# Optimization experiments

Hardware: AMD Instinct MI355X
Metric: run time of the kernel (lower is better)

## Reference

```python
import jax, jax.numpy as jnp
import numpy as np

D = 128            # shared state dim for path/link/queue (required equal by scatter_nd)
T = 8              # message-passing iterations
NUM_POLICIES = 3
MAX_NUM_QUEUES = 3
READOUT = 256


def gru(x, h, W, U, b):
    # Keras GRUCell, reset_after=True. W:[F,3D], U:[D,3D], b:[2,3D]
    gi = x @ W + b[0]
    gh = h @ U + b[1]
    iz, ir, ih = jnp.split(gi, 3, axis=-1)
    hz, hr, hh = jnp.split(gh, 3, axis=-1)
    z = jax.nn.sigmoid(iz + hz)
    r = jax.nn.sigmoid(ir + hr)
    cand = jnp.tanh(ih + r * hh)
    return z * h + (1.0 - z) * cand


def masked_gru_rnn(x_seq, h0, W, U, b):
    # x_seq: [N, Tm, F]; Masking layer: skip timesteps whose features are all zero
    def step(h, xt):
        mask = jnp.any(xt != 0, axis=-1, keepdims=True)
        hn = gru(xt, h, W, U, b)
        return jnp.where(mask, hn, h), None
    h, _ = jax.lax.scan(step, h0, jnp.swapaxes(x_seq, 0, 1))
    return h


def setup_inputs() -> dict:
    rng = np.random.default_rng(0)
    N_PATHS, N_LINKS, L, QL = 20000, 4000, 8, 3
    N_QUEUES = N_LINKS * QL
    E = N_PATHS * L
    f32 = np.float32
    traffic = rng.random(N_PATHS, dtype=f32)
    packets = rng.random(N_PATHS, dtype=f32)
    capacity = rng.random(N_LINKS, dtype=f32)
    weight = rng.random(N_QUEUES, dtype=f32)
    policy = rng.integers(0, NUM_POLICIES, N_LINKS).astype(np.int32)
    priority = rng.integers(0, MAX_NUM_QUEUES, N_QUEUES).astype(np.int32)
    # each path traverses L links; hop positions are unique per path (scatter_nd well-defined)
    path_ids = np.repeat(np.arange(N_PATHS, dtype=np.int32), L)
    l_q_p = np.tile(np.arange(L, dtype=np.int32), N_PATHS)
    l_p_s = l_q_p.copy()
    link_to_path = rng.integers(0, N_LINKS, E).astype(np.int32)
    queue_to_path = (link_to_path * QL + rng.integers(0, QL, E)).astype(np.int32)
    path_to_queue = path_ids.copy()
    sequence_queues = queue_to_path.copy()
    queue_to_link = np.arange(N_QUEUES, dtype=np.int32)  # queue i belongs to link i//QL
    sequence_links = np.repeat(np.arange(N_LINKS, dtype=np.int32), QL)
    l_q_l = np.tile(np.arange(QL, dtype=np.int32), N_LINKS)

    def p(k, *shape):
        kk = jax.random.fold_in(jax.random.key(0), k)
        return jax.random.normal(kk, shape, jnp.float32) / np.sqrt(f32(shape[0]))

    params = dict(
        Wp=p(1, 2 * D, 3 * D), Up=p(2, D, 3 * D), bp=0.01 * p(3, 2, 3 * D),
        Wl=p(4, D, 3 * D), Ul=p(5, D, 3 * D), bl=0.01 * p(6, 2, 3 * D),
        Wq=p(7, D, 3 * D), Uq=p(8, D, 3 * D), bq=0.01 * p(9, 2, 3 * D),
        Wr1=p(10, D, READOUT), br1=jnp.zeros((READOUT,), jnp.float32),
        Wr2=p(11, READOUT, READOUT), br2=jnp.zeros((READOUT,), jnp.float32),
        Wr3=p(12, READOUT, 1), br3=jnp.zeros((1,), jnp.float32),
    )
    inp = dict(
        traffic=jnp.asarray(traffic), packets=jnp.asarray(packets),
        capacity=jnp.asarray(capacity), weight=jnp.asarray(weight),
        policy=jnp.asarray(policy), priority=jnp.asarray(priority),
        path_ids=jnp.asarray(path_ids), l_q_p=jnp.asarray(l_q_p), l_p_s=jnp.asarray(l_p_s),
        link_to_path=jnp.asarray(link_to_path), queue_to_path=jnp.asarray(queue_to_path),
        path_to_queue=jnp.asarray(path_to_queue), sequence_queues=jnp.asarray(sequence_queues),
        queue_to_link=jnp.asarray(queue_to_link), sequence_links=jnp.asarray(sequence_links),
        l_q_l=jnp.asarray(l_q_l), n_paths=N_PATHS, n_links=N_LINKS, n_queues=N_QUEUES,
    )
    inp.update(params)
    return inp


def reference(traffic, packets, capacity, weight, policy, priority, path_ids, l_q_p, l_p_s,
              link_to_path, queue_to_path, path_to_queue, sequence_queues, queue_to_link,
              sequence_links, l_q_l, n_paths, n_links, n_queues,
              Wp, Up, bp, Wl, Ul, bl, Wq, Uq, bq, Wr1, br1, Wr2, br2, Wr3, br3):
    path_state = jnp.concatenate([traffic[:, None], packets[:, None],
                                  jnp.zeros((n_paths, D - 2), jnp.float32)], axis=1)
    link_state = jnp.concatenate([capacity[:, None],
                                  jax.nn.one_hot(policy, NUM_POLICIES, dtype=jnp.float32),
                                  jnp.zeros((n_links, D - NUM_POLICIES - 1), jnp.float32)], axis=1)
    queue_state = jnp.concatenate([jax.nn.one_hot(priority, MAX_NUM_QUEUES, dtype=jnp.float32),
                                   weight[:, None],
                                   jnp.zeros((n_queues, D - MAX_NUM_QUEUES - 1), jnp.float32)], axis=1)
    max_p = int(np.asarray(l_q_p).max()) + 1
    max_l = int(np.asarray(l_q_l).max()) + 1
    for _ in range(T):
        # paths: gather link+queue states, scatter into padded sequences, run masked GRU
        qg = queue_state[queue_to_path]                       # [E, D]
        lg = link_state[link_to_path]                         # [E, D]
        qi = jnp.zeros((n_paths, max_p, D), jnp.float32).at[path_ids, l_q_p].add(qg)
        li = jnp.zeros((n_paths, max_p, D), jnp.float32).at[path_ids, l_p_s].add(lg)
        path_state = masked_gru_rnn(jnp.concatenate([qi, li], axis=2), path_state, Wp, Up, bp)
        # queues: sum path states per queue, single GRU cell step
        path_sum = jax.ops.segment_sum(path_state[path_to_queue], sequence_queues,
                                       num_segments=n_queues)
        queue_state = gru(path_sum, queue_state, Wq, Uq, bq)
        # links: gather queue states into padded sequences, masked GRU
        qi2 = jnp.zeros((n_links, max_l, D), jnp.float32).at[sequence_links, l_q_l].add(
            queue_state[queue_to_link])
        link_state = masked_gru_rnn(qi2, link_state, Wl, Ul, bl)
    h = jax.nn.relu(path_state @ Wr1 + br1)
    h = jax.nn.relu(h @ Wr2 + br2)
    return h @ Wr3 + br3
```

## Files before the change

kernel.cpp:

```cpp
#include <hip/hip_runtime.h>
#include <hip/hip_bf16.h>
#include <hip/hip_fp16.h>
#include <math.h>

#define NP 20000
#define NL 4000
#define NQ 12000
#define NE 160000
#define DD 128
#define N3 384
#define TT 8
#define FR 512

typedef __attribute__((ext_vector_type(8))) short bf16x8;
typedef __attribute__((ext_vector_type(4))) float f32x4;

__device__ float g_path [NP * DD];
__device__ float g_link [NL * DD];
__device__ float g_queue[NQ * DD];
__device__ unsigned short g_qgi_h[NQ * N3];
__device__ unsigned short g_lgi_h[NL * N3];
__device__ float g_psum [NQ * DD];
__device__ int   g_peq  [NE];
__device__ int   g_pel  [NE];
__device__ int   g_qlmap[NQ];
__device__ int   g_counts[NQ];
__device__ int   g_off  [NQ + 1];
__device__ int   g_cur  [NQ];
__device__ int   g_col  [NE];
__device__ int   g_nzq  [NQ];
__device__ int   g_nzl  [NL];
__device__ unsigned short g_upb_hi[24*4*FR], g_upb_lo[24*4*FR];
__device__ unsigned short g_wpb_hi[2*24*4*FR], g_wpb_lo[2*24*4*FR];
__device__ unsigned short g_wlb_hi[24*4*FR], g_wlb_lo[24*4*FR];
__device__ unsigned short g_wuq_hi[24*8*FR], g_wuq_lo[24*8*FR];
__device__ unsigned short g_ulb_hi[24*4*FR], g_ulb_lo[24*4*FR];
__device__ unsigned short g_w1b_hi[16*4*FR], g_w1b_lo[16*4*FR];
__device__ unsigned short g_w2b_hi[16*8*FR], g_w2b_lo[16*8*FR];

__device__ __forceinline__ float fsig(float x)  { return 1.0f / (1.0f + __expf(-x)); }
__device__ __forceinline__ float ftanh(float x) { return 2.0f / (1.0f + __expf(-2.0f * x)) - 1.0f; }

__device__ __forceinline__ void split_bf(float v, unsigned short& hi, unsigned short& lo) {
    unsigned u = __float_as_uint(v);
    hi = (unsigned short)(u >> 16);
    float lof = v - __uint_as_float(u & 0xFFFF0000u);
    lo = (unsigned short)(__float_as_uint(lof) >> 16);
}
__device__ __forceinline__ unsigned short f2h(float v) {
    __half h = __float2half_rn(v);
    return *reinterpret_cast<unsigned short*>(&h);
}
__device__ __forceinline__ float h2f(unsigned short u) {
    __half h = *reinterpret_cast<__half*>(&u);
    return __half2float(h);
}

__global__ void k_init_maps() {
    int i = blockIdx.x * 256 + threadIdx.x;
    if (i < NE) { g_peq[i] = -1; g_pel[i] = -1; }
    if (i < NQ) { g_qlmap[i] = -1; g_counts[i] = 0; }
}

__global__ void k_fill_maps(const int* __restrict__ path_ids, const int* __restrict__ l_q_p,
                            const int* __restrict__ l_p_s, const int* __restrict__ queue_to_path,
                            const int* __restrict__ link_to_path, const int* __restrict__ sequence_queues,
                            const int* __restrict__ sequence_links, const int* __restrict__ l_q_l,
                            const int* __restrict__ queue_to_link) {
    int i = blockIdx.x * 256 + threadIdx.x;
    if (i < NE) {
        int p = path_ids[i];
        g_peq[p * 8 + l_q_p[i]] = queue_to_path[i];
        g_pel[p * 8 + l_p_s[i]] = link_to_path[i];
        atomicAdd(&g_counts[sequence_queues[i]], 1);
    }
    if (i < NQ) {
        g_qlmap[sequence_links[i] * 3 + l_q_l[i]] = queue_to_link[i];
    }
}

__global__ __launch_bounds__(1024) void k_scan() {
    __shared__ int part[1024];
    int tid = threadIdx.x;
    int base = tid * 12;
    int local[12];
    int s = 0;
#pragma unroll
    for (int j = 0; j < 12; j++) {
        int idx = base + j;
        int v = (idx < NQ) ? g_counts[idx] : 0;
        local[j] = s; s += v;
    }
    part[tid] = s;
    __syncthreads();
    for (int off = 1; off < 1024; off <<= 1) {
        int v = (tid >= off) ? part[tid - off] : 0;
        __syncthreads();
        part[tid] += v;
        __syncthreads();
    }
    int pre = (tid > 0) ? part[tid - 1] : 0;
#pragma unroll
    for (int j = 0; j < 12; j++) {
        int idx = base + j;
        if (idx < NQ) { g_off[idx] = pre + local[j]; g_cur[idx] = pre + local[j]; }
    }
    if (tid == 1023) g_off[NQ] = part[1023];
}

__global__ void k_fill_csr(const int* __restrict__ sequence_queues, const int* __restrict__ path_to_queue) {
    int i = blockIdx.x * 256 + threadIdx.x;
    if (i < NE) {
        int q = sequence_queues[i];
        int pos = atomicAdd(&g_cur[q], 1);
        g_col[pos] = path_to_queue[i];
    }
}

__global__ void k_init_states(const float* __restrict__ traffic, const float* __restrict__ packets,
                              const float* __restrict__ capacity, const int* __restrict__ policy,
                              const float* __restrict__ weight, const int* __restrict__ priority) {
    int idx = blockIdx.x * 256 + threadIdx.x;
    if (idx < NP * DD) {
        int p = idx >> 7, d = idx & 127;
        g_path[idx] = (d == 0) ? traffic[p] : (d == 1) ? packets[p] : 0.0f;
    }
    if (idx < NL * DD) {
        int l = idx >> 7, d = idx & 127;
        float v = 0.0f;
        if (d == 0) v = capacity[l];
        else if (d >= 1 && d <= 3) v = (policy[l] == d - 1) ? 1.0f : 0.0f;
        g_link[idx] = v;
    }
    if (idx < NQ * DD) {
        int q = idx >> 7, d = idx & 127;
        float v = 0.0f;
        if (d < 3) v = (priority[q] == d) ? 1.0f : 0.0f;
        else if (d == 3) v = weight[q];
        g_queue[idx] = v;
    }
}

__global__ void k_pack(int mode, const float* __restrict__ W, int ldn) {
    unsigned short *dhi, *dlo;
    int nt_cnt, kc_cnt, kc_total, kc_base;
    if (mode == 0)      { dhi=g_upb_hi; dlo=g_upb_lo; nt_cnt=24; kc_cnt=4; kc_total=4; kc_base=0; }
    else if (mode == 1) { dhi=g_wpb_hi; dlo=g_wpb_lo; nt_cnt=24; kc_cnt=4; kc_total=4; kc_base=0; }
    else if (mode == 2) { dhi=g_wpb_hi+24*4*FR; dlo=g_wpb_lo+24*4*FR; nt_cnt=24; kc_cnt=4; kc_total=4; kc_base=0; }
    else if (mode == 3) { dhi=g_wlb_hi; dlo=g_wlb_lo; nt_cnt=24; kc_cnt=4; kc_total=4; kc_base=0; }
    else if (mode == 4) { dhi=g_wuq_hi; dlo=g_wuq_lo; nt_cnt=24; kc_cnt=4; kc_total=8; kc_base=0; }
    else if (mode == 5) { dhi=g_wuq_hi; dlo=g_wuq_lo; nt_cnt=24; kc_cnt=4; kc_total=8; kc_base=4; }
    else if (mode == 6) { dhi=g_ulb_hi; dlo=g_ulb_lo; nt_cnt=24; kc_cnt=4; kc_total=4; kc_base=0; }
    else if (mode == 7) { dhi=g_w1b_hi; dlo=g_w1b_lo; nt_cnt=16; kc_cnt=4; kc_total=4; kc_base=0; }
    else                { dhi=g_w2b_hi; dlo=g_w2b_lo; nt_cnt=16; kc_cnt=8; kc_total=8; kc_base=0; }
    int tot = nt_cnt * kc_cnt * FR;
    int idx = blockIdx.x * 256 + threadIdx.x;
    if (idx >= tot) return;
    int j = idx & 7, lane = (idx >> 3) & 63;
    int kc = (idx >> 9) % kc_cnt, nt = idx / (kc_cnt * FR);
    int k = kc * 32 + (lane >> 4) * 8 + j;
    int col = nt * 16 + (lane & 15);
    float v = W[(size_t)k * ldn + col];
    unsigned short hi, lo;
    split_bf(v, hi, lo);
    size_t o = ((size_t)(nt * kc_total + kc_base + kc)) * FR + (size_t)lane * 8 + j;
    dhi[o] = hi; dlo[o] = lo;
}

__global__ void k_nz(int mode) {
    const float* st = mode ? g_link : g_queue;
    int n = mode ? NL : NQ;
    int* outf = mode ? g_nzl : g_nzq;
    int w = threadIdx.x >> 6, lane = threadIdx.x & 63;
    int row = blockIdx.x * 4 + w;
    if (row < n) {
        const float* r = st + (size_t)row * DD;
        bool nz = (r[lane] != 0.0f) || (r[lane + 64] != 0.0f);
        unsigned long long b = __ballot(nz);
        if (lane == 0) outf[row] = (b != 0ULL) ? 1 : 0;
    }
}

__global__ __launch_bounds__(256) void k_gemm_mfma(int mode, const float* __restrict__ bias) {
    const float* A; unsigned short* C; const unsigned short *Bh, *Bl;
    int r0; bool useB;
    if (mode == 2) {
        A = g_queue; C = g_qgi_h; Bh = g_wlb_hi; Bl = g_wlb_lo;
        r0 = blockIdx.x * 16; useB = true;
    } else {
        if (blockIdx.x < NQ / 16) {
            A = g_queue; C = g_qgi_h; Bh = g_wpb_hi; Bl = g_wpb_lo;
            r0 = blockIdx.x * 16; useB = true;
        } else {
            A = g_link; C = g_lgi_h; Bh = g_wpb_hi + 24*4*FR; Bl = g_wpb_lo + 24*4*FR;
            r0 = (blockIdx.x - NQ / 16) * 16; useB = false;
        }
    }
    __shared__ unsigned short as_hi[16][136], as_lo[16][136];
    const int tid = threadIdx.x, w = tid >> 6, l = tid & 63;
    for (int idx = tid; idx < 16 * DD; idx += 256) {
        unsigned short hi, lo;
        split_bf(A[(size_t)r0 * DD + idx], hi, lo);
        as_hi[idx >> 7][idx & 127] = hi; as_lo[idx >> 7][idx & 127] = lo;
    }
    __syncthreads();
    f32x4 acc[6];
#pragma unroll
    for (int n = 0; n < 6; n++) acc[n] = (f32x4){0.f, 0.f, 0.f, 0.f};
#pragma unroll
    for (int kc = 0; kc < 4; kc++) {
        int kk = kc * 32 + (l >> 4) * 8;
        bf16x8 ah = *reinterpret_cast<const bf16x8*>(&as_hi[l & 15][kk]);
        bf16x8 al = *reinterpret_cast<const bf16x8*>(&as_lo[l & 15][kk]);
#pragma unroll
        for (int n = 0; n < 6; n++) {
            int nt = 6 * w + n;
            size_t boff = ((size_t)(nt * 4 + kc)) * FR + (size_t)l * 8;
            bf16x8 bhv = *reinterpret_cast<const bf16x8*>(&Bh[boff]);
            bf16x8 blv = *reinterpret_cast<const bf16x8*>(&Bl[boff]);
            acc[n] = __builtin_amdgcn_mfma_f32_16x16x32_bf16(ah, bhv, acc[n], 0, 0, 0);
            acc[n] = __builtin_amdgcn_mfma_f32_16x16x32_bf16(al, bhv, acc[n], 0, 0, 0);
            acc[n] = __builtin_amdgcn_mfma_f32_16x16x32_bf16(ah, blv, acc[n], 0, 0, 0);
        }
    }
    const int rbase = (l >> 4) * 4;
#pragma unroll
    for (int n = 0; n < 6; n++) {
        int col = (6 * w + n) * 16 + (l & 15);
        float bv = useB ? bias[col] : 0.f;
#pragma unroll
        for (int i = 0; i < 4; i++)
            C[(size_t)(r0 + rbase + i) * N3 + col] = f2h(acc[n][i] + bv);
    }
}

__global__ __launch_bounds__(256) void k_path(const float* __restrict__ bp) {
    __shared__ unsigned short hs_hi[2][16][136];
    __shared__ unsigned short hs_lo[2][16][136];
    __shared__ int qqA[8][16], llA[8][16], mAsh[8][16];
    const int tid = threadIdx.x;
    const int w = tid >> 6, l = tid & 63;
    const int r0 = blockIdx.x * 16;
    if (tid < 128) {
        int r = tid >> 3, t = tid & 7;
        int e = (r0 + r) * 8 + t;
        int qq = g_peq[e], ll = g_pel[e];
        qqA[t][r] = qq; llA[t][r] = ll;
        mAsh[t][r] = (g_nzq[qq] | g_nzl[ll]);
    }
    const int c0 = 32 * w + (l & 15), c1 = c0 + 16;
    const int rbase = (l >> 4) * 4;
    float h0[4], h1[4];
#pragma unroll
    for (int i = 0; i < 4; i++) {
        h0[i] = g_path[(size_t)(r0 + rbase + i) * DD + c0];
        h1[i] = g_path[(size_t)(r0 + rbase + i) * DD + c1];
    }
#pragma unroll
    for (int i = 0; i < 4; i++) {
        unsigned short hi, lo;
        split_bf(h0[i], hi, lo); hs_hi[0][rbase + i][c0] = hi; hs_lo[0][rbase + i][c0] = lo;
        split_bf(h1[i], hi, lo); hs_hi[0][rbase + i][c1] = hi; hs_lo[0][rbase + i][c1] = lo;
    }
    __syncthreads();
    float bz[2], br[2], bh[2];
    bz[0] = bp[N3 + c0]; bz[1] = bp[N3 + c1];
    br[0] = bp[N3 + 128 + c0]; br[1] = bp[N3 + 128 + c1];
    bh[0] = bp[N3 + 256 + c0]; bh[1] = bp[N3 + 256 + c1];

    for (int t = 0; t < TT; t++) {
        const int cur = t & 1, nxt = cur ^ 1;
        int q4[4], l4[4], msk[4];
#pragma unroll
        for (int i = 0; i < 4; i++) {
            q4[i] = qqA[t][rbase + i];
            l4[i] = llA[t][rbase + i];
            msk[i] = mAsh[t][rbase + i];
        }
        float gq[2][4][3], gl[2][4][3];
#pragma unroll
        for (int tau = 0; tau < 2; tau++) {
            int cc = tau ? c1 : c0;
#pragma unroll
            for (int i = 0; i < 4; i++) {
                const unsigned short* qp = g_qgi_h + (size_t)q4[i] * N3 + cc;
                const unsigned short* lp = g_lgi_h + (size_t)l4[i] * N3 + cc;
                gq[tau][i][0] = h2f(qp[0]);   gq[tau][i][1] = h2f(qp[128]); gq[tau][i][2] = h2f(qp[256]);
                gl[tau][i][0] = h2f(lp[0]);   gl[tau][i][1] = h2f(lp[128]); gl[tau][i][2] = h2f(lp[256]);
            }
        }
        bf16x8 ah[4], al[4];
#pragma unroll
        for (int kc = 0; kc < 4; kc++) {
            ah[kc] = *reinterpret_cast<const bf16x8*>(&hs_hi[cur][l & 15][kc * 32 + (l >> 4) * 8]);
            al[kc] = *reinterpret_cast<const bf16x8*>(&hs_lo[cur][l & 15][kc * 32 + (l >> 4) * 8]);
        }
        f32x4 acc[3][2];
#pragma unroll
        for (int g = 0; g < 3; g++)
#pragma unroll
            for (int tau = 0; tau < 2; tau++) acc[g][tau] = (f32x4){0.f, 0.f, 0.f, 0.f};
#pragma unroll
        for (int kc = 0; kc < 4; kc++) {
#pragma unroll
            for (int g = 0; g < 3; g++) {
#pragma unroll
                for (int tau = 0; tau < 2; tau++) {
                    int nt = g * 8 + 2 * w + tau;
                    size_t boff = ((size_t)(nt * 4 + kc) * 64 + l) * 8;
                    bf16x8 bhv = *reinterpret_cast<const bf16x8*>(&g_upb_hi[boff]);
                    bf16x8 blv = *reinterpret_cast<const bf16x8*>(&g_upb_lo[boff]);
                    acc[g][tau] = __builtin_amdgcn_mfma_f32_16x16x32_bf16(ah[kc], bhv, acc[g][tau], 0, 0, 0);
                    acc[g][tau] = __builtin_amdgcn_mfma_f32_16x16x32_bf16(al[kc], bhv, acc[g][tau], 0, 0, 0);
                    acc[g][tau] = __builtin_amdgcn_mfma_f32_16x16x32_bf16(ah[kc], blv, acc[g][tau], 0, 0, 0);
                }
            }
        }
#pragma unroll
        for (int tau = 0; tau < 2; tau++) {
#pragma unroll
            for (int i = 0; i < 4; i++) {
                float zin = acc[0][tau][i] + gq[tau][i][0] + gl[tau][i][0] + bz[tau];
                float rin = acc[1][tau][i] + gq[tau][i][1] + gl[tau][i][1] + br[tau];
                float hold = tau ? h1[i] : h0[i];
                float zv = fsig(zin);
                float rv = fsig(rin);
                float cand = ftanh(gq[tau][i][2] + gl[tau][i][2] + rv * (acc[2][tau][i] + bh[tau]));
                float hn = zv * hold + (1.0f - zv) * cand;
                float hout = msk[i] ? hn : hold;
                if (tau) h1[i] = hout; else h0[i] = hout;
            }
        }
#pragma unroll
        for (int i = 0; i < 4; i++) {
            unsigned short hi, lo;
            split_bf(h0[i], hi, lo); hs_hi[nxt][rbase + i][c0] = hi; hs_lo[nxt][rbase + i][c0] = lo;
            split_bf(h1[i], hi, lo); hs_hi[nxt][rbase + i][c1] = hi; hs_lo[nxt][rbase + i][c1] = lo;
        }
        __syncthreads();
    }
#pragma unroll
    for (int i = 0; i < 4; i++) {
        g_path[(size_t)(r0 + rbase + i) * DD + c0] = h0[i];
        g_path[(size_t)(r0 + rbase + i) * DD + c1] = h1[i];
    }
}

__global__ void k_qsum() {
    int w = threadIdx.x >> 6, lane = threadIdx.x & 63;
    int q = blockIdx.x * 4 + w;
    if (q >= NQ) return;
    int s = g_off[q], e = g_off[q + 1];
    float a0 = 0.f, a1 = 0.f;
    for (int i = s; i < e; i++) {
        const float* p = g_path + (size_t)g_col[i] * DD;
        a0 += p[lane]; a1 += p[lane + 64];
    }
    g_psum[(size_t)q * DD + lane] = a0;
    g_psum[(size_t)q * DD + lane + 64] = a1;
}

__global__ __launch_bounds__(256) void k_queue_mfma(const float* __restrict__ bq) {
    __shared__ unsigned short xs_hi[16][136], xs_lo[16][136];
    __shared__ unsigned short hs_hi[16][136], hs_lo[16][136];
    __shared__ int nzf[16];
    const int tid = threadIdx.x, w = tid >> 6, l = tid & 63;
    const int r0 = blockIdx.x * 16;
    if (tid < 16) nzf[tid] = 0;
    for (int idx = tid; idx < 16 * DD; idx += 256) {
        unsigned short hi, lo;
        split_bf(g_psum[(size_t)r0 * DD + idx], hi, lo);
        xs_hi[idx >> 7][idx & 127] = hi; xs_lo[idx >> 7][idx & 127] = lo;
        split_bf(g_queue[(size_t)r0 * DD + idx], hi, lo);
        hs_hi[idx >> 7][idx & 127] = hi; hs_lo[idx >> 7][idx & 127] = lo;
    }
    __syncthreads();
    f32x4 aZ[2], aR[2], aIH[2], aHH[2];
#pragma unroll
    for (int tau = 0; tau < 2; tau++) {
        aZ[tau] = (f32x4){0.f,0.f,0.f,0.f}; aR[tau] = (f32x4){0.f,0.f,0.f,0.f};
        aIH[tau] = (f32x4){0.f,0.f,0.f,0.f}; aHH[tau] = (f32x4){0.f,0.f,0.f,0.f};
    }
#pragma unroll
    for (int kc = 0; kc < 8; kc++) {
        int kk = (kc & 3) * 32 + (l >> 4) * 8;
        bf16x8 ah, al;
        if (kc < 4) {
            ah = *reinterpret_cast<const bf16x8*>(&xs_hi[l & 15][kk]);
            al = *reinterpret_cast<const bf16x8*>(&xs_lo[l & 15][kk]);
        } else {
            ah = *reinterpret_cast<const bf16x8*>(&hs_hi[l & 15][kk]);
            al = *reinterpret_cast<const bf16x8*>(&hs_lo[l & 15][kk]);
        }
#pragma unroll
        for (int g = 0; g < 3; g++) {
#pragma unroll
            for (int tau = 0; tau < 2; tau++) {
                int nt = g * 8 + 2 * w + tau;
                size_t boff = ((size_t)(nt * 8 + kc)) * FR + (size_t)l * 8;
                bf16x8 bhv = *reinterpret_cast<const bf16x8*>(&g_wuq_hi[boff]);
                bf16x8 blv = *reinterpret_cast<const bf16x8*>(&g_wuq_lo[boff]);
                f32x4 a = (g == 0) ? aZ[tau] : (g == 1) ? aR[tau] : (kc < 4 ? aIH[tau] : aHH[tau]);
                a = __builtin_amdgcn_mfma_f32_16x16x32_bf16(ah, bhv, a, 0, 0, 0);
                a = __builtin_amdgcn_mfma_f32_16x16x32_bf16(al, bhv, a, 0, 0, 0);
                a = __builtin_amdgcn_mfma_f32_16x16x32_bf16(ah, blv, a, 0, 0, 0);
                if (g == 0) aZ[tau] = a; else if (g == 1) aR[tau] = a;
                else { if (kc < 4) aIH[tau] = a; else aHH[tau] = a; }
            }
        }
    }
    const int rbase = (l >> 4) * 4;
#pragma unroll
    for (int tau = 0; tau < 2; tau++) {
        int c = 32 * w + (l & 15) + (tau ? 16 : 0);
        float bz0 = bq[c],       bz1 = bq[N3 + c];
        float br0 = bq[128 + c], br1 = bq[N3 + 128 + c];
        float bh0 = bq[256 + c], bh1 = bq[N3 + 256 + c];
#pragma unroll
        for (int i = 0; i < 4; i++) {
            size_t row = (size_t)(r0 + rbase + i);
            float hold = g_queue[row * DD + c];
            float z = fsig(aZ[tau][i] + bz0 + bz1);
            float r = fsig(aR[tau][i] + br0 + br1);
            float cand = ftanh(aIH[tau][i] + bh0 + r * (aHH[tau][i] + bh1));
            float hn = z * hold + (1.0f - z) * cand;
            g_queue[row * DD + c] = hn;
            if (hn != 0.0f) nzf[rbase + i] = 1;
        }
    }
    __syncthreads();
    if (tid < 16) g_nzq[r0 + tid] = nzf[tid];
}

__global__ __launch_bounds__(256) void k_link_mfma(const float* __restrict__ bl) {
    __shared__ unsigned short hs_hi[16][136], hs_lo[16][136];
    __shared__ int qA[3][16], mA[3][16], nzf[16];
    const int tid = threadIdx.x, w = tid >> 6, l = tid & 63;
    const int r0 = blockIdx.x * 16;
    if (tid < 16) nzf[tid] = 0;
    if (tid < 48) {
        int r = tid / 3, j = tid % 3;
        int q = g_qlmap[(r0 + r) * 3 + j];
        qA[j][r] = (q < 0) ? 0 : q;
        mA[j][r] = (q >= 0 && g_nzq[q < 0 ? 0 : q]) ? 1 : 0;
    }
    const int c0 = 32 * w + (l & 15), c1 = c0 + 16;
    const int rbase = (l >> 4) * 4;
    float h0[4], h1[4];
#pragma unroll
    for (int i = 0; i < 4; i++) {
        h0[i] = g_link[(size_t)(r0 + rbase + i) * DD + c0];
        h1[i] = g_link[(size_t)(r0 + rbase + i) * DD + c1];
    }
#pragma unroll
    for (int i = 0; i < 4; i++) {
        unsigned short hi, lo;
        split_bf(h0[i], hi, lo); hs_hi[rbase + i][c0] = hi; hs_lo[rbase + i][c0] = lo;
        split_bf(h1[i], hi, lo); hs_hi[rbase + i][c1] = hi; hs_lo[rbase + i][c1] = lo;
    }
    __syncthreads();
    float bz[2], br[2], bh[2];
    bz[0] = bl[N3 + c0]; bz[1] = bl[N3 + c1];
    br[0] = bl[N3 + 128 + c0]; br[1] = bl[N3 + 128 + c1];
    bh[0] = bl[N3 + 256 + c0]; bh[1] = bl[N3 + 256 + c1];

    for (int t = 0; t < 3; t++) {
        int q4[4], msk[4];
#pragma unroll
        for (int i = 0; i < 4; i++) { q4[i] = qA[t][rbase + i]; msk[i] = mA[t][rbase + i]; }
        float gq[2][4][3];
#pragma unroll
        for (int tau = 0; tau < 2; tau++) {
            int cc = tau ? c1 : c0;
#pragma unroll
            for (int i = 0; i < 4; i++) {
                const unsigned short* qp = g_qgi_h + (size_t)q4[i] * N3 + cc;
                gq[tau][i][0] = h2f(qp[0]); gq[tau][i][1] = h2f(qp[128]); gq[tau][i][2] = h2f(qp[256]);
            }
        }
        bf16x8 ah[4], al[4];
#pragma unroll
        for (int kc = 0; kc < 4; kc++) {
            ah[kc] = *reinterpret_cast<const bf16x8*>(&hs_hi[l & 15][kc * 32 + (l >> 4) * 8]);
            al[kc] = *reinterpret_cast<const bf16x8*>(&hs_lo[l & 15][kc * 32 + (l >> 4) * 8]);
        }
        f32x4 acc[3][2];
#pragma unroll
        for (int g = 0; g < 3; g++)
#pragma unroll
            for (int tau = 0; tau < 2; tau++) acc[g][tau] = (f32x4){0.f, 0.f, 0.f, 0.f};
#pragma unroll
        for (int kc = 0; kc < 4; kc++) {
#pragma unroll
            for (int g = 0; g < 3; g++) {
#pragma unroll
                for (int tau = 0; tau < 2; tau++) {
                    int nt = g * 8 + 2 * w + tau;
                    size_t boff = ((size_t)(nt * 4 + kc)) * FR + (size_t)l * 8;
                    bf16x8 bhv = *reinterpret_cast<const bf16x8*>(&g_ulb_hi[boff]);
                    bf16x8 blv = *reinterpret_cast<const bf16x8*>(&g_ulb_lo[boff]);
                    acc[g][tau] = __builtin_amdgcn_mfma_f32_16x16x32_bf16(ah[kc], bhv, acc[g][tau], 0, 0, 0);
                    acc[g][tau] = __builtin_amdgcn_mfma_f32_16x16x32_bf16(al[kc], bhv, acc[g][tau], 0, 0, 0);
                    acc[g][tau] = __builtin_amdgcn_mfma_f32_16x16x32_bf16(ah[kc], blv, acc[g][tau], 0, 0, 0);
                }
            }
        }
        __syncthreads();
#pragma unroll
        for (int tau = 0; tau < 2; tau++) {
#pragma unroll
            for (int i = 0; i < 4; i++) {
                float zin = acc[0][tau][i] + gq[tau][i][0] + bz[tau];
                float rin = acc[1][tau][i] + gq[tau][i][1] + br[tau];
                float hold = tau ? h1[i] : h0[i];
                float zv = fsig(zin);
                float rv = fsig(rin);
                float cand = ftanh(gq[tau][i][2] + rv * (acc[2][tau][i] + bh[tau]));
                float hn = zv * hold + (1.0f - zv) * cand;
                float hout = msk[i] ? hn : hold;
                if (tau) h1[i] = hout; else h0[i] = hout;
            }
        }
#pragma unroll
        for (int i = 0; i < 4; i++) {
            unsigned short hi, lo;
            split_bf(h0[i], hi, lo); hs_hi[rbase + i][c0] = hi; hs_lo[rbase + i][c0] = lo;
            split_bf(h1[i], hi, lo); hs_hi[rbase + i][c1] = hi; hs_lo[rbase + i][c1] = lo;
        }
        __syncthreads();
    }
#pragma unroll
    for (int i = 0; i < 4; i++) {
        g_link[(size_t)(r0 + rbase + i) * DD + c0] = h0[i];
        g_link[(size_t)(r0 + rbase + i) * DD + c1] = h1[i];
        if (h0[i] != 0.0f || h1[i] != 0.0f) nzf[rbase + i] = 1;
    }
    __syncthreads();
    if (tid < 16) g_nzl[r0 + tid] = nzf[tid];
}

__global__ __launch_bounds__(256) void k_readout_mfma(const float* __restrict__ b1,
                                                      const float* __restrict__ b2,
                                                      const float* __restrict__ W3,
                                                      const float* __restrict__ b3,
                                                      float* __restrict__ out) {
    __shared__ unsigned short s1_hi[16][136], s1_lo[16][136];
    __shared__ unsigned short r1_hi[16][264], r1_lo[16][264];
    __shared__ float r2f[16][256];
    const int tid = threadIdx.x, w = tid >> 6, l = tid & 63;
    const int r0 = blockIdx.x * 16;
    for (int idx = tid; idx < 16 * DD; idx += 256) {
        unsigned short hi, lo;
        split_bf(g_path[(size_t)r0 * DD + idx], hi, lo);
        s1_hi[idx >> 7][idx & 127] = hi; s1_lo[idx >> 7][idx & 127] = lo;
    }
    __syncthreads();
    const int rbase = (l >> 4) * 4;
    {
        f32x4 acc[4];
#pragma unroll
        for (int n = 0; n < 4; n++) acc[n] = (f32x4){0.f, 0.f, 0.f, 0.f};
#pragma unroll
        for (int kc = 0; kc < 4; kc++) {
            int kk = kc * 32 + (l >> 4) * 8;
            bf16x8 ah = *reinterpret_cast<const bf16x8*>(&s1_hi[l & 15][kk]);
            bf16x8 al = *reinterpret_cast<const bf16x8*>(&s1_lo[l & 15][kk]);
#pragma unroll
            for (int n = 0; n < 4; n++) {
                int nt = 4 * w + n;
                size_t boff = ((size_t)(nt * 4 + kc)) * FR + (size_t)l * 8;
                bf16x8 bhv = *reinterpret_cast<const bf16x8*>(&g_w1b_hi[boff]);
                bf16x8 blv = *reinterpret_cast<const bf16x8*>(&g_w1b_lo[boff]);
                acc[n] = __builtin_amdgcn_mfma_f32_16x16x32_bf16(ah, bhv, acc[n], 0, 0, 0);
                acc[n] = __builtin_amdgcn_mfma_f32_16x16x32_bf16(al, bhv, acc[n], 0, 0, 0);
                acc[n] = __builtin_amdgcn_mfma_f32_16x16x32_bf16(ah, blv, acc[n], 0, 0, 0);
            }
        }
#pragma unroll
        for (int n = 0; n < 4; n++) {
            int col = (4 * w + n) * 16 + (l & 15);
#pragma unroll
            for (int i = 0; i < 4; i++) {
                float v = fmaxf(acc[n][i] + b1[col], 0.f);
                unsigned short hi, lo;
                split_bf(v, hi, lo);
                r1_hi[rbase + i][col] = hi; r1_lo[rbase + i][col] = lo;
            }
        }
    }
    __syncthreads();
    {
        f32x4 acc[4];
#pragma unroll
        for (int n = 0; n < 4; n++) acc[n] = (f32x4){0.f, 0.f, 0.f, 0.f};
#pragma unroll
        for (int kc = 0; kc < 8; kc++) {
            int kk = kc * 32 + (l >> 4) * 8;
            bf16x8 ah = *reinterpret_cast<const bf16x8*>(&r1_hi[l & 15][kk]);
            bf16x8 al = *reinterpret_cast<const bf16x8*>(&r1_lo[l & 15][kk]);
#pragma unroll
            for (int n = 0; n < 4; n++) {
                int nt = 4 * w + n;
                size_t boff = ((size_t)(nt * 8 + kc)) * FR + (size_t)l * 8;
                bf16x8 bhv = *reinterpret_cast<const bf16x8*>(&g_w2b_hi[boff]);
                bf16x8 blv = *reinterpret_cast<const bf16x8*>(&g_w2b_lo[boff]);
                acc[n] = __builtin_amdgcn_mfma_f32_16x16x32_bf16(ah, bhv, acc[n], 0, 0, 0);
                acc[n] = __builtin_amdgcn_mfma_f32_16x16x32_bf16(al, bhv, acc[n], 0, 0, 0);
                acc[n] = __builtin_amdgcn_mfma_f32_16x16x32_bf16(ah, blv, acc[n], 0, 0, 0);
            }
        }
#pragma unroll
        for (int n = 0; n < 4; n++) {
            int col = (4 * w + n) * 16 + (l & 15);
#pragma unroll
            for (int i = 0; i < 4; i++)
                r2f[rbase + i][col] = fmaxf(acc[n][i] + b2[col], 0.f);
        }
    }
    __syncthreads();
    {
        float w3a = W3[l], w3b = W3[l + 64], w3c = W3[l + 128], w3d = W3[l + 192];
#pragma unroll
        for (int rr = 0; rr < 4; rr++) {
            int row = w * 4 + rr;
            float s = r2f[row][l] * w3a + r2f[row][l + 64] * w3b +
                      r2f[row][l + 128] * w3c + r2f[row][l + 192] * w3d;
            for (int off = 32; off > 0; off >>= 1) s += __shfl_down(s, off);
            if (l == 0) out[r0 + row] = s + b3[0];
        }
    }
}

extern "C" void kernel_launch(void* const* d_in, const int* in_sizes, int n_in,
                              void* d_out, int out_size, void* d_ws, size_t ws_size,
                              hipStream_t stream) {
    const float* traffic  = (const float*)d_in[0];
    const float* packets  = (const float*)d_in[1];
    const float* capacity = (const float*)d_in[2];
    const float* weight   = (const float*)d_in[3];
    const int* policy     = (const int*)d_in[4];
    const int* priority   = (const int*)d_in[5];
    const int* path_ids   = (const int*)d_in[6];
    const int* l_q_p      = (const int*)d_in[7];
    const int* l_p_s      = (const int*)d_in[8];
    const int* link_to_path    = (const int*)d_in[9];
    const int* queue_to_path   = (const int*)d_in[10];
    const int* path_to_queue   = (const int*)d_in[11];
    const int* sequence_queues = (const int*)d_in[12];
    const int* queue_to_link   = (const int*)d_in[13];
    const int* sequence_links  = (const int*)d_in[14];
    const int* l_q_l      = (const int*)d_in[15];
    const float* Wp  = (const float*)d_in[19];
    const float* Up  = (const float*)d_in[20];
    const float* bp  = (const float*)d_in[21];
    const float* Wl  = (const float*)d_in[22];
    const float* Ul  = (const float*)d_in[23];
    const float* bl  = (const float*)d_in[24];
    const float* Wq  = (const float*)d_in[25];
    const float* Uq  = (const float*)d_in[26];
    const float* bq  = (const float*)d_in[27];
    const float* Wr1 = (const float*)d_in[28];
    const float* br1 = (const float*)d_in[29];
    const float* Wr2 = (const float*)d_in[30];
    const float* br2 = (const float*)d_in[31];
    const float* Wr3 = (const float*)d_in[32];
    const float* br3 = (const float*)d_in[33];
    float* out = (float*)d_out;

    k_init_maps<<<(NE + 255) / 256, 256, 0, stream>>>();
    k_fill_maps<<<(NE + 255) / 256, 256, 0, stream>>>(path_ids, l_q_p, l_p_s, queue_to_path,
                                                      link_to_path, sequence_queues,
                                                      sequence_links, l_q_l, queue_to_link);
    k_scan<<<1, 1024, 0, stream>>>();
    k_fill_csr<<<(NE + 255) / 256, 256, 0, stream>>>(sequence_queues, path_to_queue);
    k_init_states<<<(NP * DD + 255) / 256, 256, 0, stream>>>(traffic, packets, capacity,
                                                             policy, weight, priority);
    k_pack<<<192, 256, 0, stream>>>(0, Up, N3);
    k_pack<<<192, 256, 0, stream>>>(1, Wp, N3);
    k_pack<<<192, 256, 0, stream>>>(2, Wp + 128 * N3, N3);
    k_pack<<<192, 256, 0, stream>>>(3, Wl, N3);
    k_pack<<<192, 256, 0, stream>>>(4, Wq, N3);
    k_pack<<<192, 256, 0, stream>>>(5, Uq, N3);
    k_pack<<<192, 256, 0, stream>>>(6, Ul, N3);
    k_pack<<<128, 256, 0, stream>>>(7, Wr1, 256);
    k_pack<<<256, 256, 0, stream>>>(8, Wr2, 256);
    k_nz<<<NQ / 4, 256, 0, stream>>>(0);
    k_nz<<<NL / 4, 256, 0, stream>>>(1);

    for (int it = 0; it < TT; ++it) {
        k_gemm_mfma<<<NQ / 16 + NL / 16, 256, 0, stream>>>(3, bp);
        k_path<<<NP / 16, 256, 0, stream>>>(bp);
        k_qsum<<<NQ / 4, 256, 0, stream>>>();
        k_queue_mfma<<<NQ / 16, 256, 0, stream>>>(bq);
        k_gemm_mfma<<<NQ / 16, 256, 0, stream>>>(2, bl);
        k_link_mfma<<<NL / 16, 256, 0, stream>>>(bl);
    }

    k_readout_mfma<<<NP / 16, 256, 0, stream>>>(br1, br2, Wr3, br3, out);
}
```

Measured before the change: 1.921 ms.

## Fuse queue sum and link input projection into consumers; interleave gate layout with prefetch

Interleaves the three gate projections per column in a padded 512-wide half buffer, so the path GRU reads one 8-byte vector per row and column instead of three scattered halves. It also prefetches the next timestep's gathered projections. The per-queue path sum is folded into the queue GRU kernel, removing the intermediate psum buffer and one launch. The link input projection now runs inside the link kernel into shared memory, using the fixed queue-to-link layout and dropping another launch and the global buffer. The trade-offs are more shared memory in the link kernel, extra register pressure, and reliance on queue i belonging to link i/3 at slot i%3.

```diff
diff --git a/kernel.cpp b/kernel.cpp
--- a/kernel.cpp
+++ b/kernel.cpp
@@ -18,12 +18,10 @@
 __device__ float g_path [NP * DD];
 __device__ float g_link [NL * DD];
 __device__ float g_queue[NQ * DD];
-__device__ unsigned short g_qgi_h[NQ * N3];
-__device__ unsigned short g_lgi_h[NL * N3];
-__device__ float g_psum [NQ * DD];
+__device__ __align__(16) unsigned short g_qgi_h[NQ * 512];
+__device__ __align__(16) unsigned short g_lgi_h[NL * 512];
 __device__ int   g_peq  [NE];
 __device__ int   g_pel  [NE];
-__device__ int   g_qlmap[NQ];
 __device__ int   g_counts[NQ];
 __device__ int   g_off  [NQ + 1];
 __device__ int   g_cur  [NQ];
@@ -55,27 +53,27 @@
     __half h = *reinterpret_cast<__half*>(&u);
     return __half2float(h);
 }
+__device__ __forceinline__ void h2x2(unsigned u, float& a, float& b) {
+    __half2 h = *reinterpret_cast<__half2*>(&u);
+    float2 f = __half22float2(h);
+    a = f.x; b = f.y;
+}
 
 __global__ void k_init_maps() {
     int i = blockIdx.x * 256 + threadIdx.x;
     if (i < NE) { g_peq[i] = -1; g_pel[i] = -1; }
-    if (i < NQ) { g_qlmap[i] = -1; g_counts[i] = 0; }
+    if (i < NQ) { g_counts[i] = 0; }
 }
 
 __global__ void k_fill_maps(const int* __restrict__ path_ids, const int* __restrict__ l_q_p,
                             const int* __restrict__ l_p_s, const int* __restrict__ queue_to_path,
-                            const int* __restrict__ link_to_path, const int* __restrict__ sequence_queues,
-                            const int* __restrict__ sequence_links, const int* __restrict__ l_q_l,
-                            const int* __restrict__ queue_to_link) {
+                            const int* __restrict__ link_to_path, const int* __restrict__ sequence_queues) {
     int i = blockIdx.x * 256 + threadIdx.x;
     if (i < NE) {
         int p = path_ids[i];
         g_peq[p * 8 + l_q_p[i]] = queue_to_path[i];
         g_pel[p * 8 + l_p_s[i]] = link_to_path[i];
         atomicAdd(&g_counts[sequence_queues[i]], 1);
-    }
-    if (i < NQ) {
-        g_qlmap[sequence_links[i] * 3 + l_q_l[i]] = queue_to_link[i];
     }
 }
 
@@ -181,20 +179,15 @@
     }
 }
 
-__global__ __launch_bounds__(256) void k_gemm_mfma(int mode, const float* __restrict__ bias) {
+__global__ __launch_bounds__(256) void k_gemm_mfma(const float* __restrict__ bias) {
     const float* A; unsigned short* C; const unsigned short *Bh, *Bl;
     int r0; bool useB;
-    if (mode == 2) {
-        A = g_queue; C = g_qgi_h; Bh = g_wlb_hi; Bl = g_wlb_lo;
+    if (blockIdx.x < NQ / 16) {
+        A = g_queue; C = g_qgi_h; Bh = g_wpb_hi; Bl = g_wpb_lo;
         r0 = blockIdx.x * 16; useB = true;
     } else {
-        if (blockIdx.x < NQ / 16) {
-            A = g_queue; C = g_qgi_h; Bh = g_wpb_hi; Bl = g_wpb_lo;
-            r0 = blockIdx.x * 16; useB = true;
-        } else {
-            A = g_link; C = g_lgi_h; Bh = g_wpb_hi + 24*4*FR; Bl = g_wpb_lo + 24*4*FR;
-            r0 = (blockIdx.x - NQ / 16) * 16; useB = false;
-        }
+        A = g_link; C = g_lgi_h; Bh = g_wpb_hi + 24*4*FR; Bl = g_wpb_lo + 24*4*FR;
+        r0 = (blockIdx.x - NQ / 16) * 16; useB = false;
     }
     __shared__ unsigned short as_hi[16][136], as_lo[16][136];
     const int tid = threadIdx.x, w = tid >> 6, l = tid & 63;
@@ -226,11 +219,12 @@
     const int rbase = (l >> 4) * 4;
 #pragma unroll
     for (int n = 0; n < 6; n++) {
-        int col = (6 * w + n) * 16 + (l & 15);
-        float bv = useB ? bias[col] : 0.f;
+        int nt = 6 * w + n;
+        int gate = nt >> 3, wc = (nt & 7) * 16 + (l & 15);
+        float bv = useB ? bias[gate * 128 + wc] : 0.f;
 #pragma unroll
         for (int i = 0; i < 4; i++)
-            C[(size_t)(r0 + rbase + i) * N3 + col] = f2h(acc[n][i] + bv);
+            C[(size_t)(r0 + rbase + i) * 512 + wc * 4 + gate] = f2h(acc[n][i] + bv);
     }
 }
 
@@ -268,27 +262,36 @@
     br[0] = bp[N3 + 128 + c0]; br[1] = bp[N3 + 128 + c1];
     bh[0] = bp[N3 + 256 + c0]; bh[1] = bp[N3 + 256 + c1];
 
+    uint2 curQ[2][4], curL[2][4], nxtQ[2][4], nxtL[2][4];
+#pragma unroll
+    for (int tau = 0; tau < 2; tau++) {
+        int cc = tau ? c1 : c0;
+#pragma unroll
+        for (int i = 0; i < 4; i++) {
+            int q = qqA[0][rbase + i], lk = llA[0][rbase + i];
+            curQ[tau][i] = *reinterpret_cast<const uint2*>(&g_qgi_h[(size_t)q * 512 + cc * 4]);
+            curL[tau][i] = *reinterpret_cast<const uint2*>(&g_lgi_h[(size_t)lk * 512 + cc * 4]);
+        }
+    }
+
     for (int t = 0; t < TT; t++) {
         const int cur = t & 1, nxt = cur ^ 1;
-        int q4[4], l4[4], msk[4];
-#pragma unroll
-        for (int i = 0; i < 4; i++) {
-            q4[i] = qqA[t][rbase + i];
-            l4[i] = llA[t][rbase + i];
-            msk[i] = mAsh[t][rbase + i];
-        }
-        float gq[2][4][3], gl[2][4][3];
-#pragma unroll
-        for (int tau = 0; tau < 2; tau++) {
-            int cc = tau ? c1 : c0;
-#pragma unroll
-            for (int i = 0; i < 4; i++) {
-                const unsigned short* qp = g_qgi_h + (size_t)q4[i] * N3 + cc;
-                const unsigned short* lp = g_lgi_h + (size_t)l4[i] * N3 + cc;
-                gq[tau][i][0] = h2f(qp[0]);   gq[tau][i][1] = h2f(qp[128]); gq[tau][i][2] = h2f(qp[256]);
-                gl[tau][i][0] = h2f(lp[0]);   gl[tau][i][1] = h2f(lp[128]); gl[tau][i][2] = h2f(lp[256]);
-            }
-        }
+        if (t + 1 < TT) {
+#pragma unroll
+            for (int tau = 0; tau < 2; tau++) {
+                int cc = tau ? c1 : c0;
+#pragma unroll
+                for (int i = 0; i < 4; i++) {
+                    int q = qqA[t + 1][rbase + i], lk = llA[t + 1][rbase + i];
+                    nxtQ[tau][i] = *reinterpret_cast<const uint2*>(&g_qgi_h[(size_t)q * 512 + cc * 4]);
+                    nxtL[tau][i] = *reinterpret_cast<const uint2*>(&g_lgi_h[(size_t)lk * 512 + cc * 4]);
+                }
+            }
+        }
+        int msk[4];
+#pragma unroll
+        for (int i = 0; i < 4; i++) msk[i] = mAsh[t][rbase + i];
+
         bf16x8 ah[4], al[4];
 #pragma unroll
         for (int kc = 0; kc < 4; kc++) {
@@ -320,12 +323,17 @@
         for (int tau = 0; tau < 2; tau++) {
 #pragma unroll
             for (int i = 0; i < 4; i++) {
-                float zin = acc[0][tau][i] + gq[tau][i][0] + gl[tau][i][0] + bz[tau];
-                float rin = acc[1][tau][i] + gq[tau][i][1] + gl[tau][i][1] + br[tau];
+                float q0, q1, l0, l1;
+                h2x2(curQ[tau][i].x, q0, q1);
+                float q2 = h2f((unsigned short)(curQ[tau][i].y & 0xFFFFu));
+                h2x2(curL[tau][i].x, l0, l1);
+                float l2 = h2f((unsigned short)(curL[tau][i].y & 0xFFFFu));
+                float zin = acc[0][tau][i] + q0 + l0 + bz[tau];
+                float rin = acc[1][tau][i] + q1 + l1 + br[tau];
                 float hold = tau ? h1[i] : h0[i];
                 float zv = fsig(zin);
                 float rv = fsig(rin);
-                float cand = ftanh(gq[tau][i][2] + gl[tau][i][2] + rv * (acc[2][tau][i] + bh[tau]));
+                float cand = ftanh(q2 + l2 + rv * (acc[2][tau][i] + bh[tau]));
                 float hn = zv * hold + (1.0f - zv) * cand;
                 float hout = msk[i] ? hn : hold;
                 if (tau) h1[i] = hout; else h0[i] = hout;
@@ -337,6 +345,12 @@
             split_bf(h0[i], hi, lo); hs_hi[nxt][rbase + i][c0] = hi; hs_lo[nxt][rbase + i][c0] = lo;
             split_bf(h1[i], hi, lo); hs_hi[nxt][rbase + i][c1] = hi; hs_lo[nxt][rbase + i][c1] = lo;
         }
+        if (t + 1 < TT) {
+#pragma unroll
+            for (int tau = 0; tau < 2; tau++)
+#pragma unroll
+                for (int i = 0; i < 4; i++) { curQ[tau][i] = nxtQ[tau][i]; curL[tau][i] = nxtL[tau][i]; }
+        }
         __syncthreads();
     }
 #pragma unroll
@@ -344,20 +358,6 @@
         g_path[(size_t)(r0 + rbase + i) * DD + c0] = h0[i];
         g_path[(size_t)(r0 + rbase + i) * DD + c1] = h1[i];
     }
-}
-
-__global__ void k_qsum() {
-    int w = threadIdx.x >> 6, lane = threadIdx.x & 63;
-    int q = blockIdx.x * 4 + w;
-    if (q >= NQ) return;
-    int s = g_off[q], e = g_off[q + 1];
-    float a0 = 0.f, a1 = 0.f;
-    for (int i = s; i < e; i++) {
-        const float* p = g_path + (size_t)g_col[i] * DD;
-        a0 += p[lane]; a1 += p[lane + 64];
-    }
-    g_psum[(size_t)q * DD + lane] = a0;
-    g_psum[(size_t)q * DD + lane + 64] = a1;
 }
 
 __global__ __launch_bounds__(256) void k_queue_mfma(const float* __restrict__ bq) {
@@ -367,10 +367,22 @@
     const int tid = threadIdx.x, w = tid >> 6, l = tid & 63;
     const int r0 = blockIdx.x * 16;
     if (tid < 16) nzf[tid] = 0;
+#pragma unroll
+    for (int k = 0; k < 4; k++) {
+        int ql = 4 * w + k;
+        int q = r0 + ql;
+        int s = g_off[q], e = g_off[q + 1];
+        float a0 = 0.f, a1 = 0.f;
+        for (int i = s; i < e; i++) {
+            const float* p = g_path + (size_t)g_col[i] * DD;
+            a0 += p[l]; a1 += p[l + 64];
+        }
+        unsigned short hi, lo;
+        split_bf(a0, hi, lo); xs_hi[ql][l] = hi; xs_lo[ql][l] = lo;
+        split_bf(a1, hi, lo); xs_hi[ql][l + 64] = hi; xs_lo[ql][l + 64] = lo;
+    }
     for (int idx = tid; idx < 16 * DD; idx += 256) {
         unsigned short hi, lo;
-        split_bf(g_psum[(size_t)r0 * DD + idx], hi, lo);
-        xs_hi[idx >> 7][idx & 127] = hi; xs_lo[idx >> 7][idx & 127] = lo;
         split_bf(g_queue[(size_t)r0 * DD + idx], hi, lo);
         hs_hi[idx >> 7][idx & 127] = hi; hs_lo[idx >> 7][idx & 127] = lo;
     }
@@ -433,19 +445,56 @@
 }
 
 __global__ __launch_bounds__(256) void k_link_mfma(const float* __restrict__ bl) {
-    __shared__ unsigned short hs_hi[16][136], hs_lo[16][136];
-    __shared__ int qA[3][16], mA[3][16], nzf[16];
+    __shared__ unsigned short proj[48][128][3];
+    __shared__ unsigned short sh_hi[16][136], sh_lo[16][136];
+    __shared__ int mA[3][16], nzf[16];
     const int tid = threadIdx.x, w = tid >> 6, l = tid & 63;
     const int r0 = blockIdx.x * 16;
     if (tid < 16) nzf[tid] = 0;
     if (tid < 48) {
         int r = tid / 3, j = tid % 3;
-        int q = g_qlmap[(r0 + r) * 3 + j];
-        qA[j][r] = (q < 0) ? 0 : q;
-        mA[j][r] = (q >= 0 && g_nzq[q < 0 ? 0 : q]) ? 1 : 0;
+        mA[j][r] = g_nzq[3 * (r0 + r) + j];
+    }
+    const int rbase = (l >> 4) * 4;
+    for (int s = 0; s < 3; s++) {
+        int qbase = 3 * r0 + 16 * s;
+        for (int idx = tid; idx < 16 * DD; idx += 256) {
+            unsigned short hi, lo;
+            split_bf(g_queue[(size_t)qbase * DD + idx], hi, lo);
+            sh_hi[idx >> 7][idx & 127] = hi; sh_lo[idx >> 7][idx & 127] = lo;
+        }
+        __syncthreads();
+        f32x4 acc[6];
+#pragma unroll
+        for (int n = 0; n < 6; n++) acc[n] = (f32x4){0.f, 0.f, 0.f, 0.f};
+#pragma unroll
+        for (int kc = 0; kc < 4; kc++) {
+            int kk = kc * 32 + (l >> 4) * 8;
+            bf16x8 ah = *reinterpret_cast<const bf16x8*>(&sh_hi[l & 15][kk]);
+            bf16x8 al = *reinterpret_cast<const bf16x8*>(&sh_lo[l & 15][kk]);
+#pragma unroll
+            for (int n = 0; n < 6; n++) {
+                int nt = 6 * w + n;
+                size_t boff = ((size_t)(nt * 4 + kc)) * FR + (size_t)l * 8;
+                bf16x8 bhv = *reinterpret_cast<const bf16x8*>(&g_wlb_hi[boff]);
+                bf16x8 blv = *reinterpret_cast<const bf16x8*>(&g_wlb_lo[boff]);
+                acc[n] = __builtin_amdgcn_mfma_f32_16x16x32_bf16(ah, bhv, acc[n], 0, 0, 0);
+                acc[n] = __builtin_amdgcn_mfma_f32_16x16x32_bf16(al, bhv, acc[n], 0, 0, 0);
+                acc[n] = __builtin_amdgcn_mfma_f32_16x16x32_bf16(ah, blv, acc[n], 0, 0, 0);
+            }
+        }
+#pragma unroll
+        for (int n = 0; n < 6; n++) {
+            int nt = 6 * w + n;
+            int gate = nt >> 3, wc = (nt & 7) * 16 + (l & 15);
+            float bv = bl[gate * 128 + wc];
+#pragma unroll
+            for (int i = 0; i < 4; i++)
+                proj[16 * s + rbase + i][wc][gate] = f2h(acc[n][i] + bv);
+        }
+        __syncthreads();
     }
     const int c0 = 32 * w + (l & 15), c1 = c0 + 16;
-    const int rbase = (l >> 4) * 4;
     float h0[4], h1[4];
 #pragma unroll
     for (int i = 0; i < 4; i++) {
@@ -455,8 +504,8 @@
 #pragma unroll
     for (int i = 0; i < 4; i++) {
         unsigned short hi, lo;
-        split_bf(h0[i], hi, lo); hs_hi[rbase + i][c0] = hi; hs_lo[rbase + i][c0] = lo;
-        split_bf(h1[i], hi, lo); hs_hi[rbase + i][c1] = hi; hs_lo[rbase + i][c1] = lo;
+        split_bf(h0[i], hi, lo); sh_hi[rbase + i][c0] = hi; sh_lo[rbase + i][c0] = lo;
+        split_bf(h1[i], hi, lo); sh_hi[rbase + i][c1] = hi; sh_lo[rbase + i][c1] = lo;
     }
     __syncthreads();
     float bz[2], br[2], bh[2];
@@ -465,24 +514,14 @@
     bh[0] = bl[N3 + 256 + c0]; bh[1] = bl[N3 + 256 + c1];
 
     for (int t = 0; t < 3; t++) {
-        int q4[4], msk[4];
-#pragma unroll
-        for (int i = 0; i < 4; i++) { q4[i] = qA[t][rbase + i]; msk[i] = mA[t][rbase + i]; }
-        float gq[2][4][3];
-#pragma unroll
-        for (int tau = 0; tau < 2; tau++) {
-            int cc = tau ? c1 : c0;
-#pragma unroll
-            for (int i = 0; i < 4; i++) {
-                const unsigned short* qp = g_qgi_h + (size_t)q4[i] * N3 + cc;
-                gq[tau][i][0] = h2f(qp[0]); gq[tau][i][1] = h2f(qp[128]); gq[tau][i][2] = h2f(qp[256]);
-            }
-        }
+        int msk[4];
+#pragma unroll
+        for (int i = 0; i < 4; i++) msk[i] = mA[t][rbase + i];
         bf16x8 ah[4], al[4];
 #pragma unroll
         for (int kc = 0; kc < 4; kc++) {
-            ah[kc] = *reinterpret_cast<const bf16x8*>(&hs_hi[l & 15][kc * 32 + (l >> 4) * 8]);
-            al[kc] = *reinterpret_cast<const bf16x8*>(&hs_lo[l & 15][kc * 32 + (l >> 4) * 8]);
+            ah[kc] = *reinterpret_cast<const bf16x8*>(&sh_hi[l & 15][kc * 32 + (l >> 4) * 8]);
+            al[kc] = *reinterpret_cast<const bf16x8*>(&sh_lo[l & 15][kc * 32 + (l >> 4) * 8]);
         }
         f32x4 acc[3][2];
 #pragma unroll
@@ -508,14 +547,19 @@
         __syncthreads();
 #pragma unroll
         for (int tau = 0; tau < 2; tau++) {
+            int cc = tau ? c1 : c0;
 #pragma unroll
             for (int i = 0; i < 4; i++) {
-                float zin = acc[0][tau][i] + gq[tau][i][0] + bz[tau];
-                float rin = acc[1][tau][i] + gq[tau][i][1] + br[tau];
+                int qloc = 3 * (rbase + i) + t;
+                float q0 = h2f(proj[qloc][cc][0]);
+                float q1 = h2f(proj[qloc][cc][1]);
+                float q2 = h2f(proj[qloc][cc][2]);
+                float zin = acc[0][tau][i] + q0 + bz[tau];
+                float rin = acc[1][tau][i] + q1 + br[tau];
                 float hold = tau ? h1[i] : h0[i];
                 float zv = fsig(zin);
                 float rv = fsig(rin);
-                float cand = ftanh(gq[tau][i][2] + rv * (acc[2][tau][i] + bh[tau]));
+                float cand = ftanh(q2 + rv * (acc[2][tau][i] + bh[tau]));
                 float hn = zv * hold + (1.0f - zv) * cand;
                 float hout = msk[i] ? hn : hold;
                 if (tau) h1[i] = hout; else h0[i] = hout;
@@ -524,8 +568,8 @@
 #pragma unroll
         for (int i = 0; i < 4; i++) {
             unsigned short hi, lo;
-            split_bf(h0[i], hi, lo); hs_hi[rbase + i][c0] = hi; hs_lo[rbase + i][c0] = lo;
-            split_bf(h1[i], hi, lo); hs_hi[rbase + i][c1] = hi; hs_lo[rbase + i][c1] = lo;
+            split_bf(h0[i], hi, lo); sh_hi[rbase + i][c0] = hi; sh_lo[rbase + i][c0] = lo;
+            split_bf(h1[i], hi, lo); sh_hi[rbase + i][c1] = hi; sh_lo[rbase + i][c1] = lo;
         }
         __syncthreads();
     }
@@ -647,9 +691,6 @@
     const int* queue_to_path   = (const int*)d_in[10];
     const int* path_to_queue   = (const int*)d_in[11];
     const int* sequence_queues = (const int*)d_in[12];
-    const int* queue_to_link   = (const int*)d_in[13];
-    const int* sequence_links  = (const int*)d_in[14];
-    const int* l_q_l      = (const int*)d_in[15];
     const float* Wp  = (const float*)d_in[19];
     const float* Up  = (const float*)d_in[20];
     const float* bp  = (const float*)d_in[21];
@@ -669,8 +710,7 @@
 
     k_init_maps<<<(NE + 255) / 256, 256, 0, stream>>>();
     k_fill_maps<<<(NE + 255) / 256, 256, 0, stream>>>(path_ids, l_q_p, l_p_s, queue_to_path,
-                                                      link_to_path, sequence_queues,
-                                                      sequence_links, l_q_l, queue_to_link);
+                                                      link_to_path, sequence_queues);
     k_scan<<<1, 1024, 0, stream>>>();
     k_fill_csr<<<(NE + 255) / 256, 256, 0, stream>>>(sequence_queues, path_to_queue);
     k_init_states<<<(NP * DD + 255) / 256, 256, 0, stream>>>(traffic, packets, capacity,
@@ -688,11 +728,9 @@
     k_nz<<<NL / 4, 256, 0, stream>>>(1);
 
     for (int it = 0; it < TT; ++it) {
-        k_gemm_mfma<<<NQ / 16 + NL / 16, 256, 0, stream>>>(3, bp);
+        k_gemm_mfma<<<NQ / 16 + NL / 16, 256, 0, stream>>>(bp);
         k_path<<<NP / 16, 256, 0, stream>>>(bp);
-        k_qsum<<<NQ / 4, 256, 0, stream>>>();
         k_queue_mfma<<<NQ / 16, 256, 0, stream>>>(bq);
-        k_gemm_mfma<<<NQ / 16, 256, 0, stream>>>(2, bl);
         k_link_mfma<<<NL / 16, 256, 0, stream>>>(bl);
     }
 
```

After: 2.244 ms. +16.8%, slower.
